# Performance work log

Measured on AMD Instinct MI355X. Metric: run time of the kernel, lower is better.

## Reference

```python
import jax, jax.numpy as jnp
import numpy as np

B, S, HID = 2, 2048, 2048
H, D_NOPE, D_ROPE = 16, 128, 64
KV_LORA = 192            # forced so v_head dim == pad_hd == 128 (see torch view)
NUM_SLOTS, MAX_LEN = 8, 2048
SCALE = D_NOPE ** -0.5


def setup_inputs() -> dict:
    key = jax.random.key(0)
    ks = jax.random.split(key, 4)
    return {
        "hidden_states": jax.random.normal(ks[0], (B, S, HID), jnp.float32),
        "Wq": jax.random.normal(ks[1], (H * (D_NOPE + D_ROPE), HID), jnp.float32) * 0.02,
        "Wkv": jax.random.normal(ks[2], (KV_LORA + D_ROPE, HID), jnp.float32) * 0.02,
        "Wo": jax.random.normal(ks[3], (HID, H * D_NOPE), jnp.float32) * 0.02,
        "k_cache": jnp.zeros((NUM_SLOTS, MAX_LEN, 1, D_NOPE), jnp.float32),
        "v_cache": jnp.zeros((NUM_SLOTS, MAX_LEN, 1, D_NOPE), jnp.float32),
        "slot_mapping": jnp.arange(B, dtype=jnp.int32),
        "kv_start_indices": jnp.zeros((B,), jnp.int32),
        "seq_lens": jnp.full((B,), S, jnp.int32),
        "positions": jnp.arange(S, dtype=jnp.int32),
    }


def reference(hidden_states, Wq, Wkv, Wo, k_cache, v_cache,
              slot_mapping, kv_start_indices, seq_lens, positions):
    # q / low-rank kv projections (nn.Linear convention: x @ W.T)
    q = (hidden_states @ Wq.T).reshape(B, S, H, D_NOPE + D_ROPE)
    q_nope = q[..., :D_NOPE]                       # [B,S,H,128]
    kv = hidden_states @ Wkv.T                     # [B,S,256]
    k = kv[..., :D_NOPE][:, :, None, :]            # [B,S,1,128] single latent kv head
    v = kv[..., D_NOPE:][:, :, None, :]            # [B,S,1,128]

    # paged KV-cache scatter (prefill: kv_start_indices == 0, write [0:S))
    k_cache = k_cache.at[slot_mapping, :S].set(k)
    v_cache = v_cache.at[slot_mapping, :S].set(v)

    # gather history back (max_l = seq_lens.max() == S at prefill, static)
    k_hist = k_cache[slot_mapping, :S]             # [B,L,1,128]
    v_hist = v_cache[slot_mapping, :S]

    # MQA attention: sum over singleton kv-head axis == repeat_interleave broadcast
    scores = jnp.einsum('bshd,blod->bhsl', q_nope, k_hist) * SCALE  # [B,H,S,L]
    causal = jnp.triu(jnp.ones((S, S), bool), k=1)  # diagonal = start(0)+1
    scores = jnp.where(causal[None, None], -jnp.inf, scores)
    attn = jax.nn.softmax(scores, axis=-1)
    out = jnp.einsum('bhsl,blod->bshd', attn, v_hist)  # [B,S,H,128]
    out = out.reshape(B, S, H * D_NOPE)
    return out @ Wo.T
```

## Files before the change

kernel.cpp:

```cpp
#include <hip/hip_runtime.h>
#include <hip/hip_bf16.h>
#include <stdint.h>


typedef __attribute__((ext_vector_type(4))) float f32x4;
typedef __attribute__((ext_vector_type(8))) short bf16x8;
typedef __attribute__((ext_vector_type(4))) short bf16x4;
typedef __attribute__((ext_vector_type(8))) unsigned short u16x8;

__device__ __forceinline__ unsigned short f2bf(float f) {
    union { float f; unsigned u; } v; v.f = f;
    unsigned u = v.u;
    return (unsigned short)((u + 0x7fffu + ((u >> 16) & 1u)) >> 16);
}

__device__ __forceinline__ short bf_rn(float f) {
    __hip_bfloat16 h = __float2bfloat16(f);
    short s; __builtin_memcpy(&s, &h, 2); return s;
}

__device__ __forceinline__ float exp2_raw(float x) {
#if __has_builtin(__builtin_amdgcn_exp2f)
    return __builtin_amdgcn_exp2f(x);
#else
    return exp2f(x);
#endif
}

#define MFMA32(a,b,c) __builtin_amdgcn_mfma_f32_16x16x32_bf16((a),(b),(c),0,0,0)
#if defined(__HIP_DEVICE_COMPILE__)
#define MFMA16(a,b,c) __builtin_amdgcn_mfma_f32_16x16x16bf16_1k((a),(b),(c),0,0,0)
#else
#define MFMA16(a,b,c) (c)
#endif

#define GLD_LDS16(g,l) __builtin_amdgcn_global_load_lds( \
    (const __attribute__((address_space(1))) unsigned int*)(g), \
    (__attribute__((address_space(3))) unsigned int*)(l), 16, 0, 0)

__device__ __forceinline__ u16x8 cvt8(const float4 a, const float4 b, float sc) {
    u16x8 r;
    r[0] = f2bf(a.x * sc); r[1] = f2bf(a.y * sc);
    r[2] = f2bf(a.z * sc); r[3] = f2bf(a.w * sc);
    r[4] = f2bf(b.x * sc); r[5] = f2bf(b.y * sc);
    r[6] = f2bf(b.z * sc); r[7] = f2bf(b.w * sc);
    return r;
}

__global__ void cvt_fused(const float* __restrict__ hs, const float* __restrict__ wo,
                          const float* __restrict__ wq, const float* __restrict__ wkv,
                          unsigned short* __restrict__ h_bf,
                          unsigned short* __restrict__ wo_bf,
                          unsigned short* __restrict__ wqkv_bf) {
    const int bid = blockIdx.x;
    if (bid < 993) {
        const int stride = 993 * 256;
        for (int i = bid * 256 + threadIdx.x; i < 1048576; i += stride) {
            float4 a = ((const float4*)hs)[2 * i];
            float4 b = ((const float4*)hs)[2 * i + 1];
            ((u16x8*)h_bf)[i] = cvt8(a, b, 1.0f);
        }
    } else if (bid < 1490) {
        const int stride = 497 * 256;
        for (int i = (bid - 993) * 256 + threadIdx.x; i < 524288; i += stride) {
            float4 a = ((const float4*)wo)[2 * i];
            float4 b = ((const float4*)wo)[2 * i + 1];
            ((u16x8*)wo_bf)[i] = cvt8(a, b, 1.0f);
        }
    } else {
        const int stride = 558 * 256;
        for (int i = (bid - 1490) * 256 + threadIdx.x; i < 589824; i += stride) {
            const int row = i >> 8;
            const int col = i & 255;
            const bool isq = (row < 2048);
            const float sc = isq ? 0.1275174331181861f : 1.0f;
            const float* srcp = isq ? (wq + (long)((row >> 7) * 192 + (row & 127)) * 2048)
                                    : (wkv + (long)(row - 2048) * 2048);
            float4 a = ((const float4*)srcp)[2 * col];
            float4 b = ((const float4*)srcp)[2 * col + 1];
            ((u16x8*)(wqkv_bf + (long)row * 2048))[col] = cvt8(a, b, sc);
        }
    }
}

__global__ void transpose_v(const unsigned short* __restrict__ qkv, unsigned short* __restrict__ vt) {
    __shared__ unsigned short tile[32][33];
    const int b = blockIdx.z, dt = blockIdx.y, st = blockIdx.x;
    const int x = threadIdx.x, y = threadIdx.y;
    const int s0 = st * 32, d0 = dt * 32;
    #pragma unroll
    for (int i = 0; i < 4; ++i)
        tile[y + i * 8][x] = qkv[((long)(b * 2048 + s0 + y + i * 8)) * 2304 + 2176 + d0 + x];
    __syncthreads();
    #pragma unroll
    for (int i = 0; i < 4; ++i)
        vt[((long)(b * 128 + d0 + y + i * 8)) * 2048 + s0 + x] = tile[x][y + i * 8];
}

template<int OUT_BF16>
__global__ __launch_bounds__(256, 2)
void gemm_bt(const unsigned short* __restrict__ A,
             const unsigned short* __restrict__ B,
             void* __restrict__ Cp, int M, int N, int K) {
    __shared__ unsigned short As[128 * 64];
    __shared__ unsigned short Bs[128 * 64];
    const int t = threadIdx.x;
    const int wave = t >> 6, lane = t & 63;
    const int wr = wave >> 1, wc = wave & 1;
    const int l15 = lane & 15, l4 = lane >> 4;

    const int nbx = gridDim.x;
    const int nwg = nbx * gridDim.y;
    const int borig = blockIdx.y * nbx + blockIdx.x;
    const int bswz = (borig & 7) * (nwg >> 3) + (borig >> 3);
    const long m0 = (bswz / nbx) * 128L, n0 = (bswz % nbx) * 128L;

    const unsigned short* asrc[4];
    const unsigned short* bsrc[4];
    #pragma unroll
    for (int it = 0; it < 4; ++it) {
        const int c = it * 4 + wave;
        const int row = c * 8 + (lane >> 3);
        const int gsw = (lane & 7) ^ (row & 7);
        asrc[it] = A + (m0 + row) * K + gsw * 8;
        bsrc[it] = B + (n0 + row) * K + gsw * 8;
    }

    f32x4 acc[4][4] = {};
    for (int k0 = 0; k0 < K; k0 += 64) {
        #pragma unroll
        for (int it = 0; it < 4; ++it) {
            const int c = it * 4 + wave;
            GLD_LDS16(asrc[it] + k0, As + c * 512);
            GLD_LDS16(bsrc[it] + k0, Bs + c * 512);
        }
        __syncthreads();
        #pragma unroll
        for (int ks = 0; ks < 2; ++ks) {
            bf16x8 af[4], bfr[4];
            #pragma unroll
            for (int m = 0; m < 4; ++m) {
                const int row = wr * 64 + m * 16 + l15;
                const int slot = (ks * 4 + l4) ^ (row & 7);
                af[m] = *(const bf16x8*)(As + row * 64 + slot * 8);
            }
            #pragma unroll
            for (int n = 0; n < 4; ++n) {
                const int row = wc * 64 + n * 16 + l15;
                const int slot = (ks * 4 + l4) ^ (row & 7);
                bfr[n] = *(const bf16x8*)(Bs + row * 64 + slot * 8);
            }
            #pragma unroll
            for (int m = 0; m < 4; ++m)
                #pragma unroll
                for (int n = 0; n < 4; ++n)
                    acc[m][n] = MFMA32(af[m], bfr[n], acc[m][n]);
        }
        __syncthreads();
    }

    #pragma unroll
    for (int m = 0; m < 4; ++m)
        #pragma unroll
        for (int n = 0; n < 4; ++n) {
            const long rg = m0 + wr * 64 + m * 16 + l4 * 4;
            const long cg = n0 + wc * 64 + n * 16 + l15;
            #pragma unroll
            for (int i = 0; i < 4; ++i) {
                float v = acc[m][n][i];
                if (OUT_BF16) ((unsigned short*)Cp)[(rg + i) * N + cg] = f2bf(v);
                else          ((float*)Cp)[(rg + i) * N + cg] = v;
            }
        }
}

__global__ __launch_bounds__(256, 2)
void attn_fused(const unsigned short* __restrict__ QKV,
                const unsigned short* __restrict__ VT,
                unsigned short* __restrict__ AO) {
    __shared__ unsigned short Ks[2][64 * 128];
    __shared__ unsigned short Vs[2][128 * 64];
    const int t = threadIdx.x;
    const int wave = t >> 6, lane = t & 63;
    const int l15 = lane & 15, l4 = lane >> 4;
    const int bid = blockIdx.x;
    const int p = bid >> 4;
    const int hgb = bid & 15;
    const int hg = hgb >> 1, b = hgb & 1;
    const int h = hg * 2 + (wave >> 1);
    const int qsub = wave & 1;
    const long rowB = (long)b * 2048;

    const unsigned short* ksrc[4];
    const unsigned short* vsrc[4];
    #pragma unroll
    for (int it = 0; it < 4; ++it) {
        const int c = it * 4 + wave;
        const int krow = c * 4 + (lane >> 4);
        const int ksp = (lane & 15) ^ (krow & 15);
        ksrc[it] = QKV + (rowB + krow) * 2304 + 2048 + ksp * 8;
        const int vd = c * 8 + (lane >> 3);
        const int vsp = (lane & 7) ^ (vd & 7);
        vsrc[it] = VT + ((long)b * 128 + vd) * 2048 + vsp * 8;
    }

#define STAGE(bufi, jj0) do { \
    _Pragma("unroll") \
    for (int it = 0; it < 4; ++it) { \
        const int c = it * 4 + wave; \
        GLD_LDS16(ksrc[it] + (long)(jj0) * 2304, &Ks[bufi][c * 512]); \
        GLD_LDS16(vsrc[it] + (jj0), &Vs[bufi][c * 512]); \
    } \
} while (0)

    for (int ph = 0; ph < 2; ++ph) {
        const int qt = ph ? p : (63 - p);
        const int q0 = qt * 32;
        const int q0w = q0 + qsub * 16;
        const int nt = (qt >> 1) + 1;

        bf16x8 qf[4];
        {
            const unsigned short* qp = QKV + (rowB + q0w + l15) * 2304 + h * 128;
            #pragma unroll
            for (int kb = 0; kb < 4; ++kb)
                qf[kb] = *(const bf16x8*)(qp + kb * 32 + l4 * 8);
        }

        f32x4 o[8] = {};
        float lsum = 0.f;

        STAGE(0, 0);
        int cur = 0;

        for (int tt = 0; tt < nt; ++tt) {
            const int j0 = tt * 64;
            asm volatile("s_waitcnt vmcnt(0)" ::: "memory");
            __builtin_amdgcn_s_barrier();
            if (tt + 1 < nt) STAGE(cur ^ 1, j0 + 64);

            const unsigned short* ksBase = cur ? &Ks[1][0] : &Ks[0][0];
            f32x4 st[4];
            __builtin_amdgcn_s_setprio(1);
            #pragma unroll
            for (int jkv = 0; jkv < 4; ++jkv) {
                const unsigned short* krp = ksBase + (jkv * 16 + l15) * 128;
                f32x4 s0 = {};
                #pragma unroll
                for (int kb = 0; kb < 4; ++kb) {
                    const int slot = (kb * 4 + l4) ^ l15;
                    bf16x8 kf = *(const bf16x8*)(krp + slot * 8);
                    s0 = MFMA32(kf, qf[kb], s0);
                }
                st[jkv] = s0;
            }
            __builtin_amdgcn_s_setprio(0);

            if (tt + 1 == nt) {
                const int qrow = q0w + l15;
                #pragma unroll
                for (int jkv = 0; jkv < 4; ++jkv)
                    #pragma unroll
                    for (int i = 0; i < 4; ++i) {
                        const int kpos = j0 + jkv * 16 + l4 * 4 + i;
                        if (kpos > qrow) st[jkv][i] = -3.0e38f;
                    }
            }
            float ps = 0.f;
            bf16x4 pa[4];
            #pragma unroll
            for (int jkv = 0; jkv < 4; ++jkv) {
                float p0 = exp2_raw(st[jkv][0]);
                float p1 = exp2_raw(st[jkv][1]);
                float p2 = exp2_raw(st[jkv][2]);
                float p3 = exp2_raw(st[jkv][3]);
                ps += (p0 + p1) + (p2 + p3);
#if defined(__HIP_DEVICE_COMPILE__)
                unsigned r0, r1;
                asm("v_cvt_pk_bf16_f32 %0, %1, %2" : "=v"(r0) : "v"(p0), "v"(p1));
                asm("v_cvt_pk_bf16_f32 %0, %1, %2" : "=v"(r1) : "v"(p2), "v"(p3));
                union { unsigned u[2]; bf16x4 v; } cvt;
                cvt.u[0] = r0; cvt.u[1] = r1;
                pa[jkv] = cvt.v;
#else
                bf16x4 v = { bf_rn(p0), bf_rn(p1), bf_rn(p2), bf_rn(p3) };
                pa[jkv] = v;
#endif
            }
            lsum += ps;

            const unsigned short* vsBase = cur ? &Vs[1][0] : &Vs[0][0];
            __builtin_amdgcn_s_setprio(1);
            #pragma unroll
            for (int dj = 0; dj < 8; ++dj) {
                const int d = dj * 16 + l15;
                const unsigned short* vrow = vsBase + d * 64;
                const int dsw = (d & 7) << 3;
                #pragma unroll
                for (int jkv = 0; jkv < 4; ++jkv) {
                    bf16x4 vf = *(const bf16x4*)(vrow + ((jkv * 16 + l4 * 4) ^ dsw));
                    o[dj] = MFMA16(pa[jkv], vf, o[dj]);
                }
            }
            __builtin_amdgcn_s_setprio(0);
            cur ^= 1;
        }

        float lrow = lsum;
        lrow += __shfl_xor(lrow, 16);
        lrow += __shfl_xor(lrow, 32);
        float il[4];
        #pragma unroll
        for (int i = 0; i < 4; ++i)
            il[i] = 1.0f / __shfl(lrow, l4 * 4 + i);
        #pragma unroll
        for (int dj = 0; dj < 8; ++dj)
            #pragma unroll
            for (int i = 0; i < 4; ++i) {
                const long qrow = rowB + q0w + l4 * 4 + i;
                AO[qrow * 2048 + h * 128 + dj * 16 + l15] = (unsigned short)bf_rn(o[dj][i] * il[i]);
            }
        __syncthreads();
    }
#undef STAGE
}

extern "C" void kernel_launch(void* const* d_in, const int* in_sizes, int n_in,
                              void* d_out, int out_size, void* d_ws, size_t ws_size,
                              hipStream_t stream) {
    const float* hs  = (const float*)d_in[0];
    const float* Wq  = (const float*)d_in[1];
    const float* Wkv = (const float*)d_in[2];
    const float* Wo  = (const float*)d_in[3];
    char* ws = (char*)d_ws;
    unsigned short* h_bf   = (unsigned short*)(ws + 0);
    unsigned short* wqkv_bf= (unsigned short*)(ws + 16777216);
    unsigned short* wo_bf  = (unsigned short*)(ws + 26214400);
    unsigned short* qkv_bf = (unsigned short*)(ws + 34603008);
    unsigned short* vt_bf  = (unsigned short*)(ws + 53477376);
    unsigned short* ao_bf  = (unsigned short*)(ws + 54525952);
    float* out = (float*)d_out;

    cvt_fused<<<2048, 256, 0, stream>>>(hs, Wo, Wq, Wkv, h_bf, wo_bf, wqkv_bf);

    gemm_bt<1><<<dim3(18, 32), 256, 0, stream>>>(h_bf, wqkv_bf, qkv_bf, 4096, 2304, 2048);
    transpose_v<<<dim3(64, 4, 2), dim3(32, 8), 0, stream>>>(qkv_bf, vt_bf);
    attn_fused<<<dim3(512, 1, 1), 256, 0, stream>>>(qkv_bf, vt_bf, ao_bf);
    gemm_bt<0><<<dim3(16, 32), 256, 0, stream>>>(ao_bf, wo_bf, out, 4096, 2048, 2048);
}
```

Before: 166.6 us.

## Single-buffer V tile and split attention into one q-tile per block

V in shared memory drops from double to single buffering, so each block needs less LDS and launch bounds rise to three blocks per CU. The two-phase pairing of a heavy and a light q-tile per block is replaced by one q-tile per block, doubling the grid and launching the heaviest tiles first. The V prefetch is moved to after the PV MFMAs, behind an extra barrier, and waits use partial vmcnt counts. The aim is more resident waves to hide latency, at the cost of less overlap of V loads and more per-block setup.

Result: no change. 167.4 us (+0.5%).

```diff
diff --git a/kernel.cpp b/kernel.cpp
--- a/kernel.cpp
+++ b/kernel.cpp
@@ -174,22 +174,25 @@
         }
 }
 
-__global__ __launch_bounds__(256, 2)
+__global__ __launch_bounds__(256, 3)
 void attn_fused(const unsigned short* __restrict__ QKV,
                 const unsigned short* __restrict__ VT,
                 unsigned short* __restrict__ AO) {
     __shared__ unsigned short Ks[2][64 * 128];
-    __shared__ unsigned short Vs[2][128 * 64];
+    __shared__ unsigned short Vs[128 * 64];
     const int t = threadIdx.x;
     const int wave = t >> 6, lane = t & 63;
     const int l15 = lane & 15, l4 = lane >> 4;
     const int bid = blockIdx.x;
-    const int p = bid >> 4;
+    const int qt = 63 - (bid >> 4);
     const int hgb = bid & 15;
     const int hg = hgb >> 1, b = hgb & 1;
     const int h = hg * 2 + (wave >> 1);
     const int qsub = wave & 1;
     const long rowB = (long)b * 2048;
+    const int q0 = qt * 32;
+    const int q0w = q0 + qsub * 16;
+    const int nt = (qt >> 1) + 1;
 
     const unsigned short* ksrc[4];
     const unsigned short* vsrc[4];
@@ -204,125 +207,134 @@
         vsrc[it] = VT + ((long)b * 128 + vd) * 2048 + vsp * 8;
     }
 
-#define STAGE(bufi, jj0) do { \
+#define STAGE_K(bufi, jj0) do { \
     _Pragma("unroll") \
     for (int it = 0; it < 4; ++it) { \
         const int c = it * 4 + wave; \
         GLD_LDS16(ksrc[it] + (long)(jj0) * 2304, &Ks[bufi][c * 512]); \
-        GLD_LDS16(vsrc[it] + (jj0), &Vs[bufi][c * 512]); \
     } \
 } while (0)
 
-    for (int ph = 0; ph < 2; ++ph) {
-        const int qt = ph ? p : (63 - p);
-        const int q0 = qt * 32;
-        const int q0w = q0 + qsub * 16;
-        const int nt = (qt >> 1) + 1;
-
-        bf16x8 qf[4];
-        {
-            const unsigned short* qp = QKV + (rowB + q0w + l15) * 2304 + h * 128;
-            #pragma unroll
-            for (int kb = 0; kb < 4; ++kb)
-                qf[kb] = *(const bf16x8*)(qp + kb * 32 + l4 * 8);
-        }
-
-        f32x4 o[8] = {};
-        float lsum = 0.f;
-
-        STAGE(0, 0);
-        int cur = 0;
-
-        for (int tt = 0; tt < nt; ++tt) {
-            const int j0 = tt * 64;
-            asm volatile("s_waitcnt vmcnt(0)" ::: "memory");
-            __builtin_amdgcn_s_barrier();
-            if (tt + 1 < nt) STAGE(cur ^ 1, j0 + 64);
-
-            const unsigned short* ksBase = cur ? &Ks[1][0] : &Ks[0][0];
-            f32x4 st[4];
-            __builtin_amdgcn_s_setprio(1);
+#define STAGE_V(jj0) do { \
+    _Pragma("unroll") \
+    for (int it = 0; it < 4; ++it) { \
+        const int c = it * 4 + wave; \
+        GLD_LDS16(vsrc[it] + (jj0), &Vs[c * 512]); \
+    } \
+} while (0)
+
+    bf16x8 qf[4];
+    {
+        const unsigned short* qp = QKV + (rowB + q0w + l15) * 2304 + h * 128;
+        #pragma unroll
+        for (int kb = 0; kb < 4; ++kb)
+            qf[kb] = *(const bf16x8*)(qp + kb * 32 + l4 * 8);
+    }
+
+    f32x4 o[8] = {};
+    float lsum = 0.f;
+
+    STAGE_K(0, 0);
+    STAGE_V(0);
+    asm volatile("s_waitcnt vmcnt(0)" ::: "memory");
+    __builtin_amdgcn_s_barrier();
+    int cur = 0;
+
+    for (int tt = 0; tt < nt; ++tt) {
+        const int j0 = tt * 64;
+        const bool pf = (tt + 1 < nt);
+        if (pf) STAGE_K(cur ^ 1, j0 + 64);
+
+        const unsigned short* ksBase = cur ? &Ks[1][0] : &Ks[0][0];
+        f32x4 st[4];
+        __builtin_amdgcn_s_setprio(1);
+        #pragma unroll
+        for (int jkv = 0; jkv < 4; ++jkv) {
+            const unsigned short* krp = ksBase + (jkv * 16 + l15) * 128;
+            f32x4 s0 = {};
+            #pragma unroll
+            for (int kb = 0; kb < 4; ++kb) {
+                const int slot = (kb * 4 + l4) ^ l15;
+                bf16x8 kf = *(const bf16x8*)(krp + slot * 8);
+                s0 = MFMA32(kf, qf[kb], s0);
+            }
+            st[jkv] = s0;
+        }
+        __builtin_amdgcn_s_setprio(0);
+
+        if (tt + 1 == nt) {
+            const int qrow = q0w + l15;
+            #pragma unroll
+            for (int jkv = 0; jkv < 4; ++jkv)
+                #pragma unroll
+                for (int i = 0; i < 4; ++i) {
+                    const int kpos = j0 + jkv * 16 + l4 * 4 + i;
+                    if (kpos > qrow) st[jkv][i] = -3.0e38f;
+                }
+        }
+        float ps = 0.f;
+        bf16x4 pa[4];
+        #pragma unroll
+        for (int jkv = 0; jkv < 4; ++jkv) {
+            float p0 = exp2_raw(st[jkv][0]);
+            float p1 = exp2_raw(st[jkv][1]);
+            float p2 = exp2_raw(st[jkv][2]);
+            float p3 = exp2_raw(st[jkv][3]);
+            ps += (p0 + p1) + (p2 + p3);
+#if defined(__HIP_DEVICE_COMPILE__)
+            unsigned r0, r1;
+            asm("v_cvt_pk_bf16_f32 %0, %1, %2" : "=v"(r0) : "v"(p0), "v"(p1));
+            asm("v_cvt_pk_bf16_f32 %0, %1, %2" : "=v"(r1) : "v"(p2), "v"(p3));
+            union { unsigned u[2]; bf16x4 v; } cvt;
+            cvt.u[0] = r0; cvt.u[1] = r1;
+            pa[jkv] = cvt.v;
+#else
+            bf16x4 v = { bf_rn(p0), bf_rn(p1), bf_rn(p2), bf_rn(p3) };
+            pa[jkv] = v;
+#endif
+        }
+        lsum += ps;
+
+        if (pf) asm volatile("s_waitcnt vmcnt(4)" ::: "memory");
+        else    asm volatile("s_waitcnt vmcnt(0)" ::: "memory");
+        __builtin_amdgcn_s_barrier();
+
+        __builtin_amdgcn_s_setprio(1);
+        #pragma unroll
+        for (int dj = 0; dj < 8; ++dj) {
+            const int d = dj * 16 + l15;
+            const unsigned short* vrow = &Vs[d * 64];
+            const int dsw = (d & 7) << 3;
             #pragma unroll
             for (int jkv = 0; jkv < 4; ++jkv) {
-                const unsigned short* krp = ksBase + (jkv * 16 + l15) * 128;
-                f32x4 s0 = {};
-                #pragma unroll
-                for (int kb = 0; kb < 4; ++kb) {
-                    const int slot = (kb * 4 + l4) ^ l15;
-                    bf16x8 kf = *(const bf16x8*)(krp + slot * 8);
-                    s0 = MFMA32(kf, qf[kb], s0);
-                }
-                st[jkv] = s0;
-            }
-            __builtin_amdgcn_s_setprio(0);
-
-            if (tt + 1 == nt) {
-                const int qrow = q0w + l15;
-                #pragma unroll
-                for (int jkv = 0; jkv < 4; ++jkv)
-                    #pragma unroll
-                    for (int i = 0; i < 4; ++i) {
-                        const int kpos = j0 + jkv * 16 + l4 * 4 + i;
-                        if (kpos > qrow) st[jkv][i] = -3.0e38f;
-                    }
-            }
-            float ps = 0.f;
-            bf16x4 pa[4];
-            #pragma unroll
-            for (int jkv = 0; jkv < 4; ++jkv) {
-                float p0 = exp2_raw(st[jkv][0]);
-                float p1 = exp2_raw(st[jkv][1]);
-                float p2 = exp2_raw(st[jkv][2]);
-                float p3 = exp2_raw(st[jkv][3]);
-                ps += (p0 + p1) + (p2 + p3);
-#if defined(__HIP_DEVICE_COMPILE__)
-                unsigned r0, r1;
-                asm("v_cvt_pk_bf16_f32 %0, %1, %2" : "=v"(r0) : "v"(p0), "v"(p1));
-                asm("v_cvt_pk_bf16_f32 %0, %1, %2" : "=v"(r1) : "v"(p2), "v"(p3));
-                union { unsigned u[2]; bf16x4 v; } cvt;
-                cvt.u[0] = r0; cvt.u[1] = r1;
-                pa[jkv] = cvt.v;
-#else
-                bf16x4 v = { bf_rn(p0), bf_rn(p1), bf_rn(p2), bf_rn(p3) };
-                pa[jkv] = v;
-#endif
-            }
-            lsum += ps;
-
-            const unsigned short* vsBase = cur ? &Vs[1][0] : &Vs[0][0];
-            __builtin_amdgcn_s_setprio(1);
-            #pragma unroll
-            for (int dj = 0; dj < 8; ++dj) {
-                const int d = dj * 16 + l15;
-                const unsigned short* vrow = vsBase + d * 64;
-                const int dsw = (d & 7) << 3;
-                #pragma unroll
-                for (int jkv = 0; jkv < 4; ++jkv) {
-                    bf16x4 vf = *(const bf16x4*)(vrow + ((jkv * 16 + l4 * 4) ^ dsw));
-                    o[dj] = MFMA16(pa[jkv], vf, o[dj]);
-                }
-            }
-            __builtin_amdgcn_s_setprio(0);
-            cur ^= 1;
-        }
-
-        float lrow = lsum;
-        lrow += __shfl_xor(lrow, 16);
-        lrow += __shfl_xor(lrow, 32);
-        float il[4];
-        #pragma unroll
-        for (int i = 0; i < 4; ++i)
-            il[i] = 1.0f / __shfl(lrow, l4 * 4 + i);
-        #pragma unroll
-        for (int dj = 0; dj < 8; ++dj)
-            #pragma unroll
-            for (int i = 0; i < 4; ++i) {
-                const long qrow = rowB + q0w + l4 * 4 + i;
-                AO[qrow * 2048 + h * 128 + dj * 16 + l15] = (unsigned short)bf_rn(o[dj][i] * il[i]);
-            }
-        __syncthreads();
-    }
-#undef STAGE
+                bf16x4 vf = *(const bf16x4*)(vrow + ((jkv * 16 + l4 * 4) ^ dsw));
+                o[dj] = MFMA16(pa[jkv], vf, o[dj]);
+            }
+        }
+        __builtin_amdgcn_s_setprio(0);
+
+        asm volatile("s_waitcnt vmcnt(0)" ::: "memory");
+        __builtin_amdgcn_s_barrier();
+        if (pf) STAGE_V(j0 + 64);
+        cur ^= 1;
+    }
+
+    float lrow = lsum;
+    lrow += __shfl_xor(lrow, 16);
+    lrow += __shfl_xor(lrow, 32);
+    float il[4];
+    #pragma unroll
+    for (int i = 0; i < 4; ++i)
+        il[i] = 1.0f / __shfl(lrow, l4 * 4 + i);
+    #pragma unroll
+    for (int dj = 0; dj < 8; ++dj)
+        #pragma unroll
+        for (int i = 0; i < 4; ++i) {
+            const long qrow = rowB + q0w + l4 * 4 + i;
+            AO[qrow * 2048 + h * 128 + dj * 16 + l15] = (unsigned short)bf_rn(o[dj][i] * il[i]);
+        }
+#undef STAGE_K
+#undef STAGE_V
 }
 
 extern "C" void kernel_launch(void* const* d_in, const int* in_sizes, int n_in,
@@ -345,6 +357,6 @@
 
     gemm_bt<1><<<dim3(18, 32), 256, 0, stream>>>(h_bf, wqkv_bf, qkv_bf, 4096, 2304, 2048);
     transpose_v<<<dim3(64, 4, 2), dim3(32, 8), 0, stream>>>(qkv_bf, vt_bf);
-    attn_fused<<<dim3(512, 1, 1), 256, 0, stream>>>(qkv_bf, vt_bf, ao_bf);
+    attn_fused<<<dim3(1024, 1, 1), 256, 0, stream>>>(qkv_bf, vt_bf, ao_bf);
     gemm_bt<0><<<dim3(16, 32), 256, 0, stream>>>(ao_bf, wo_bf, out, 4096, 2048, 2048);
 }
```
